# Kernel tuning notes

Measured on AMD Instinct MI355X. Metric: run time of the kernel, lower is better.

Reference implementation:

```python
import jax, jax.numpy as jnp
import numpy as np

B, T, D = 128, 1024, 128

def setup_inputs() -> dict:
    key = jax.random.key(0)
    k1, k2 = jax.random.split(key)
    x = jax.random.normal(k1, (B, T, 3 * D), dtype=jnp.float32)
    # original init: kernel = gain * eye(d_dim); use eye plus small noise for a nontrivial test
    kernel = jnp.eye(D, dtype=jnp.float32) + 0.01 * jax.random.normal(k2, (D, D), dtype=jnp.float32)
    return {"x": x, "kernel": kernel}

def reference(x, kernel):
    d = kernel.shape[0]
    # x: (B, T, 3d) -> channel blocks (module permutes to (B,C,T) then back; net effect is slicing last dim)
    y = x[:, :, :d]            # (B, T, d) observed values
    w = x[:, :, d:2 * d]       # (B, T, d) log-intensities
    y_obs = x[:, :, 2 * d:3 * d]  # (B, T, d) transient targets
    intensity = jnp.exp(w)
    # softmax across channels per timestep (exp(w - logsumexp_d w))
    sm = jax.nn.softmax(w, axis=2)
    mean = jnp.mean(y, axis=1, keepdims=True)  # (B, 1, d), broadcast over T
    # cross-channel mixing: small per-timestep d x d matmul
    smooth = jnp.matmul(sm * (y - mean), kernel) + mean  # (B, T, d)
    y_trans = y_obs - smooth
    # concat order matches torch.cat([rep1, intensity, y_trans], dim=1) after final permute
    return jnp.concatenate([smooth, intensity, y_trans], axis=-1)  # (B, T, 3d)
```

## Files before the change

### kernel.cpp

```cpp
#include <hip/hip_runtime.h>
#include <cstdint>

#define D_CH 128
#define T_LEN 1024
#define ROWLEN 384
#define NROWS (128 * 1024)
#define TILE 64
#define NCHUNK (NROWS / TILE)
#define KSTRIDE 136

typedef __attribute__((ext_vector_type(8))) _Float16 f16x8;
typedef __attribute__((ext_vector_type(4))) _Float16 f16x4;
typedef __attribute__((ext_vector_type(4))) float f32x4;

__global__ __launch_bounds__(256) void prep_kernel(const float* __restrict__ x,
                                                   const float* __restrict__ Kmat,
                                                   float* __restrict__ meang,
                                                   _Float16* __restrict__ Ktg) {
  int bid = blockIdx.x;
  int b = bid >> 1, h = bid & 1;
  int tid = threadIdx.x;
  int li = tid & 15, tt = tid >> 4;
  int d4 = h * 64 + 4 * li;
  float4 s = make_float4(0.f, 0.f, 0.f, 0.f);
  const float* xp = x + (size_t)b * T_LEN * ROWLEN + d4;
#pragma unroll 4
  for (int j = 0; j < 64; ++j) {
    int t = tt + 16 * j;
    float4 v = *(const float4*)(xp + (size_t)t * ROWLEN);
    s.x += v.x; s.y += v.y; s.z += v.z; s.w += v.w;
  }
  __shared__ float4 red[16][17];
  red[tt][li] = s;
  __syncthreads();
  for (int st = 8; st > 0; st >>= 1) {
    if (tt < st) {
      float4 o = red[tt + st][li];
      float4 m = red[tt][li];
      m.x += o.x; m.y += o.y; m.z += o.z; m.w += o.w;
      red[tt][li] = m;
    }
    __syncthreads();
  }
  if (tt == 0) {
    float4 m = red[0][li];
    const float inv = 1.0f / 1024.0f;
    m.x *= inv; m.y *= inv; m.z *= inv; m.w *= inv;
    *(float4*)(meang + b * D_CH + d4) = m;
  }
  if (tid < 64) {
    int idx = bid * 64 + tid;
    int n = idx >> 7, k = idx & 127;
    Ktg[idx] = (_Float16)Kmat[k * D_CH + n];
  }
}

__global__ __launch_bounds__(256, 3) void main_kernel(const float* __restrict__ x,
                                                      const float* __restrict__ meang,
                                                      const _Float16* __restrict__ Ktg,
                                                      float* __restrict__ out) {
  __shared__ _Float16 Kt[D_CH * KSTRIDE];
  __shared__ _Float16 vs[TILE * KSTRIDE];
  int tid = threadIdx.x;
  {
    const uint32_t* kw = (const uint32_t*)Ktg;
    uint32_t* kl = (uint32_t*)Kt;
#pragma unroll
    for (int i = 0; i < 32; ++i) {
      int widx = tid + i * 256;
      int n = widx >> 6, k2 = widx & 63;
      kl[n * (KSTRIDE / 2) + k2] = kw[widx];
    }
  }
  __syncthreads();

  int wave = tid >> 6, lane = tid & 63;
  int hf = lane >> 5, li = lane & 31;
  int c0 = 4 * li;
  int m0 = wave * 16;
  int l15 = lane & 15, lg = lane >> 4;
  int abase = (m0 + l15) * KSTRIDE + lg * 8;
  int bbase = l15 * KSTRIDE + lg * 8;

  for (int chunk = blockIdx.x; chunk < NCHUNK; chunk += gridDim.x) {
    int row0 = chunk * TILE;
    int bb = chunk >> 4;
    const float* mb = meang + bb * D_CH;

    float4 yb[8], wb[8];
#pragma unroll
    for (int i = 0; i < 8; ++i) {
      size_t base = (size_t)(row0 + m0 + 2 * i + hf) * ROWLEN + c0;
      yb[i] = *(const float4*)(x + base);
      wb[i] = *(const float4*)(x + base + 128);
    }
    float4 mn = *(const float4*)(mb + c0);
#pragma unroll
    for (int i = 0; i < 8; ++i) {
      int rl = m0 + 2 * i + hf;
      int row = row0 + rl;
      float4 e;
      e.x = __expf(wb[i].x); e.y = __expf(wb[i].y);
      e.z = __expf(wb[i].z); e.w = __expf(wb[i].w);
      *(float4*)(out + (size_t)row * ROWLEN + 128 + c0) = e;
      float s = e.x + e.y + e.z + e.w;
      s += __shfl_xor(s, 1, 32);
      s += __shfl_xor(s, 2, 32);
      s += __shfl_xor(s, 4, 32);
      s += __shfl_xor(s, 8, 32);
      s += __shfl_xor(s, 16, 32);
      float rinv = 1.0f / s;
      f16x4 vh;
      vh[0] = (_Float16)(e.x * rinv * (yb[i].x - mn.x));
      vh[1] = (_Float16)(e.y * rinv * (yb[i].y - mn.y));
      vh[2] = (_Float16)(e.z * rinv * (yb[i].z - mn.z));
      vh[3] = (_Float16)(e.w * rinv * (yb[i].w - mn.w));
      *(f16x4*)&vs[rl * KSTRIDE + c0] = vh;
    }

    f16x8 a[4];
#pragma unroll
    for (int ks = 0; ks < 4; ++ks)
      a[ks] = *(const f16x8*)&vs[abase + ks * 32];
#pragma unroll
    for (int nt = 0; nt < 8; ++nt) {
      f32x4 acc = {0.f, 0.f, 0.f, 0.f};
#pragma unroll
      for (int ks = 0; ks < 4; ++ks) {
        f16x8 bf = *(const f16x8*)&Kt[bbase + nt * 16 * KSTRIDE + ks * 32];
        acc = __builtin_amdgcn_mfma_f32_16x16x32_f16(a[ks], bf, acc, 0, 0, 0);
      }
      int col = nt * 16 + l15;
      float mcol = mb[col];
#pragma unroll
      for (int r = 0; r < 4; ++r) {
        int row = row0 + m0 + lg * 4 + r;
        size_t ob = (size_t)row * ROWLEN;
        float sm = acc[r] + mcol;
        out[ob + col] = sm;
        out[ob + 256 + col] = x[ob + 256 + col] - sm;
      }
    }
  }
}

extern "C" void kernel_launch(void* const* d_in, const int* in_sizes, int n_in,
                              void* d_out, int out_size, void* d_ws, size_t ws_size,
                              hipStream_t stream) {
  const float* x = (const float*)d_in[0];
  const float* Kmat = (const float*)d_in[1];
  float* out = (float*)d_out;
  float* meang = (float*)d_ws;
  _Float16* Ktg = (_Float16*)((char*)d_ws + 65536);
  prep_kernel<<<256, 256, 0, stream>>>(x, Kmat, meang, Ktg);
  main_kernel<<<1024, 256, 0, stream>>>(x, meang, Ktg, out);
}
```

Before: 355.8 us.

## Pre-swizzle K into MFMA fragment order, drop LDS K staging, vectorize epilogue

The prep kernel now writes K in the exact per-lane MFMA B-fragment order, so the main kernel loads B fragments straight from global/L2 instead of staging a 128x128 K tile in LDS per block. Each block handles one 64-row chunk (grid = NCHUNK) with per-wave LDS slices and no block barrier. The output stage goes through an LDS transpose, so the smooth and y_trans columns are written and y_obs is read as coalesced float4 rows instead of scalar strided accesses. The trade-off is more blocks and repeated global reads of K per wave, which depend on cache hits.

```diff
diff --git a/kernel.cpp b/kernel.cpp
--- a/kernel.cpp
+++ b/kernel.cpp
@@ -7,7 +7,10 @@
 #define NROWS (128 * 1024)
 #define TILE 64
 #define NCHUNK (NROWS / TILE)
-#define KSTRIDE 136
+#define VSTR_B 272
+#define VS_SLICE (16 * VSTR_B)
+#define EPI_W 132
+#define EPI_SLICE (16 * EPI_W * 4)
 
 typedef __attribute__((ext_vector_type(8))) _Float16 f16x8;
 typedef __attribute__((ext_vector_type(4))) _Float16 f16x4;
@@ -49,9 +52,14 @@
     *(float4*)(meang + b * D_CH + d4) = m;
   }
   if (tid < 64) {
-    int idx = bid * 64 + tid;
-    int n = idx >> 7, k = idx & 127;
-    Ktg[idx] = (_Float16)Kmat[k * D_CH + n];
+    int f = bid * 64 + tid;
+    int j = f & 7;
+    int lane = (f >> 3) & 63;
+    int q = f >> 9;
+    int ks = q & 3, nt = q >> 2;
+    int kk = ks * 32 + (lane >> 4) * 8 + j;
+    int nn = nt * 16 + (lane & 15);
+    Ktg[f] = (_Float16)Kmat[kk * D_CH + nn];
   }
 }
 
@@ -59,88 +67,86 @@
                                                       const float* __restrict__ meang,
                                                       const _Float16* __restrict__ Ktg,
                                                       float* __restrict__ out) {
-  __shared__ _Float16 Kt[D_CH * KSTRIDE];
-  __shared__ _Float16 vs[TILE * KSTRIDE];
+  __shared__ alignas(16) char vsbuf[4 * VS_SLICE];
+  __shared__ alignas(16) char epibuf[4 * EPI_SLICE];
   int tid = threadIdx.x;
-  {
-    const uint32_t* kw = (const uint32_t*)Ktg;
-    uint32_t* kl = (uint32_t*)Kt;
-#pragma unroll
-    for (int i = 0; i < 32; ++i) {
-      int widx = tid + i * 256;
-      int n = widx >> 6, k2 = widx & 63;
-      kl[n * (KSTRIDE / 2) + k2] = kw[widx];
-    }
-  }
-  __syncthreads();
-
   int wave = tid >> 6, lane = tid & 63;
   int hf = lane >> 5, li = lane & 31;
   int c0 = 4 * li;
   int m0 = wave * 16;
   int l15 = lane & 15, lg = lane >> 4;
-  int abase = (m0 + l15) * KSTRIDE + lg * 8;
-  int bbase = l15 * KSTRIDE + lg * 8;
+  char* vslice = vsbuf + wave * VS_SLICE;
+  float* epi = (float*)(epibuf + wave * EPI_SLICE);
 
-  for (int chunk = blockIdx.x; chunk < NCHUNK; chunk += gridDim.x) {
-    int row0 = chunk * TILE;
-    int bb = chunk >> 4;
-    const float* mb = meang + bb * D_CH;
+  int chunk = blockIdx.x;
+  int row0 = chunk * TILE;
+  int bb = chunk >> 4;
+  const float* mb = meang + bb * D_CH;
+  float4 mn = *(const float4*)(mb + c0);
 
-    float4 yb[8], wb[8];
+  float4 yb[8], wb[8];
 #pragma unroll
-    for (int i = 0; i < 8; ++i) {
-      size_t base = (size_t)(row0 + m0 + 2 * i + hf) * ROWLEN + c0;
-      yb[i] = *(const float4*)(x + base);
-      wb[i] = *(const float4*)(x + base + 128);
+  for (int i = 0; i < 8; ++i) {
+    size_t base = (size_t)(row0 + m0 + 2 * i + hf) * ROWLEN + c0;
+    yb[i] = *(const float4*)(x + base);
+    wb[i] = *(const float4*)(x + base + 128);
+  }
+#pragma unroll
+  for (int i = 0; i < 8; ++i) {
+    int lr = 2 * i + hf;
+    int row = row0 + m0 + lr;
+    float4 e;
+    e.x = __expf(wb[i].x); e.y = __expf(wb[i].y);
+    e.z = __expf(wb[i].z); e.w = __expf(wb[i].w);
+    *(float4*)(out + (size_t)row * ROWLEN + 128 + c0) = e;
+    float s = e.x + e.y + e.z + e.w;
+    s += __shfl_xor(s, 1, 32);
+    s += __shfl_xor(s, 2, 32);
+    s += __shfl_xor(s, 4, 32);
+    s += __shfl_xor(s, 8, 32);
+    s += __shfl_xor(s, 16, 32);
+    float rinv = 1.0f / s;
+    f16x4 vh;
+    vh[0] = (_Float16)(e.x * rinv * (yb[i].x - mn.x));
+    vh[1] = (_Float16)(e.y * rinv * (yb[i].y - mn.y));
+    vh[2] = (_Float16)(e.z * rinv * (yb[i].z - mn.z));
+    vh[3] = (_Float16)(e.w * rinv * (yb[i].w - mn.w));
+    *(f16x4*)(vslice + lr * VSTR_B + li * 8) = vh;
+  }
+
+  f16x8 a[4];
+#pragma unroll
+  for (int ks = 0; ks < 4; ++ks)
+    a[ks] = *(const f16x8*)(vslice + l15 * VSTR_B + ks * 64 + lg * 16);
+  f32x4 acc[8];
+#pragma unroll
+  for (int nt = 0; nt < 8; ++nt) {
+    acc[nt] = (f32x4){0.f, 0.f, 0.f, 0.f};
+#pragma unroll
+    for (int ks = 0; ks < 4; ++ks) {
+      f16x8 bf = *(const f16x8*)&Ktg[((nt * 4 + ks) * 64 + lane) * 8];
+      acc[nt] = __builtin_amdgcn_mfma_f32_16x16x32_f16(a[ks], bf, acc[nt], 0, 0, 0);
     }
-    float4 mn = *(const float4*)(mb + c0);
+  }
+
 #pragma unroll
-    for (int i = 0; i < 8; ++i) {
-      int rl = m0 + 2 * i + hf;
-      int row = row0 + rl;
-      float4 e;
-      e.x = __expf(wb[i].x); e.y = __expf(wb[i].y);
-      e.z = __expf(wb[i].z); e.w = __expf(wb[i].w);
-      *(float4*)(out + (size_t)row * ROWLEN + 128 + c0) = e;
-      float s = e.x + e.y + e.z + e.w;
-      s += __shfl_xor(s, 1, 32);
-      s += __shfl_xor(s, 2, 32);
-      s += __shfl_xor(s, 4, 32);
-      s += __shfl_xor(s, 8, 32);
-      s += __shfl_xor(s, 16, 32);
-      float rinv = 1.0f / s;
-      f16x4 vh;
-      vh[0] = (_Float16)(e.x * rinv * (yb[i].x - mn.x));
-      vh[1] = (_Float16)(e.y * rinv * (yb[i].y - mn.y));
-      vh[2] = (_Float16)(e.z * rinv * (yb[i].z - mn.z));
-      vh[3] = (_Float16)(e.w * rinv * (yb[i].w - mn.w));
-      *(f16x4*)&vs[rl * KSTRIDE + c0] = vh;
-    }
+  for (int nt = 0; nt < 8; ++nt)
+#pragma unroll
+    for (int r = 0; r < 4; ++r)
+      epi[(lg * 4 + r) * EPI_W + nt * 16 + l15] = acc[nt][r];
 
-    f16x8 a[4];
 #pragma unroll
-    for (int ks = 0; ks < 4; ++ks)
-      a[ks] = *(const f16x8*)&vs[abase + ks * 32];
-#pragma unroll
-    for (int nt = 0; nt < 8; ++nt) {
-      f32x4 acc = {0.f, 0.f, 0.f, 0.f};
-#pragma unroll
-      for (int ks = 0; ks < 4; ++ks) {
-        f16x8 bf = *(const f16x8*)&Kt[bbase + nt * 16 * KSTRIDE + ks * 32];
-        acc = __builtin_amdgcn_mfma_f32_16x16x32_f16(a[ks], bf, acc, 0, 0, 0);
-      }
-      int col = nt * 16 + l15;
-      float mcol = mb[col];
-#pragma unroll
-      for (int r = 0; r < 4; ++r) {
-        int row = row0 + m0 + lg * 4 + r;
-        size_t ob = (size_t)row * ROWLEN;
-        float sm = acc[r] + mcol;
-        out[ob + col] = sm;
-        out[ob + 256 + col] = x[ob + 256 + col] - sm;
-      }
-    }
+  for (int i = 0; i < 8; ++i) {
+    int lr = 2 * i + hf;
+    size_t ob = (size_t)(row0 + m0 + lr) * ROWLEN;
+    float4 sm4 = *(const float4*)&epi[lr * EPI_W + c0];
+    sm4.x += mn.x; sm4.y += mn.y; sm4.z += mn.z; sm4.w += mn.w;
+    float4 yo = *(const float4*)(x + ob + 256 + c0);
+    *(float4*)(out + ob + c0) = sm4;
+    float4 yt;
+    yt.x = yo.x - sm4.x; yt.y = yo.y - sm4.y;
+    yt.z = yo.z - sm4.z; yt.w = yo.w - sm4.w;
+    *(float4*)(out + ob + 256 + c0) = yt;
   }
 }
 
@@ -153,5 +159,5 @@
   float* meang = (float*)d_ws;
   _Float16* Ktg = (_Float16*)((char*)d_ws + 65536);
   prep_kernel<<<256, 256, 0, stream>>>(x, Kmat, meang, Ktg);
-  main_kernel<<<1024, 256, 0, stream>>>(x, meang, Ktg, out);
+  main_kernel<<<NCHUNK, 256, 0, stream>>>(x, meang, Ktg, out);
 }
```

Measured after the change: 350.5 us. No clear change (-1.5%).
